# Kernel tuning notes

Hardware: AMD Instinct MI355X
Metric: run time of the kernel (lower is better)

## Reference

```python
import jax, jax.numpy as jnp
import numpy as np


def _rank_transform_ascending(flat):
    # torch: _, idx = sort(flat, descending=False); flat[idx] = linspace(0,1,n)+1/n
    n = flat.shape[0]
    order = jnp.argsort(flat)  # ascending
    prob = jnp.linspace(0.0, 1.0, n, dtype=flat.dtype) + jnp.asarray(1.0 / n, flat.dtype)
    return jnp.zeros_like(flat).at[order].set(prob)


def corr_attention(query, key, value):
    # score[b,h,i,j] = cosine-like similarity q_i . k_j / (|q_i| |k_j|)
    score = jnp.einsum('bhid,bhjd->bhij', query, key)
    q_len = jnp.sqrt(jnp.sum(query * query, axis=-1, keepdims=True)) + 1e-5  # [b,h,s,1]
    k_len = jnp.sqrt(jnp.sum(key * key, axis=-1, keepdims=True)) + 1e-5      # [b,h,s,1]
    score = score / (q_len * jnp.swapaxes(k_len, -1, -2))
    signal = jnp.sign(score)
    size = score.shape
    flat = jnp.abs(score).reshape(-1)
    ranked = _rank_transform_ascending(flat)
    score = -jnp.log(ranked).reshape(size) * signal
    score = score / jnp.sum(jnp.abs(score), axis=-1, keepdims=True)
    return jnp.einsum('bhij,bhjd->bhid', score, value)


def setup_inputs() -> dict:
    key0 = jax.random.key(0)
    kq, kk, kv = jax.random.split(key0, 3)
    B, H, S, D = 4, 8, 1024, 64
    query = jax.random.normal(kq, (B, H, S, D), dtype=jnp.float32)
    key = jax.random.normal(kk, (B, H, S, D), dtype=jnp.float32)
    value = jax.random.normal(kv, (B, H, S, D), dtype=jnp.float32)
    return {"query": query, "key": key, "value": value}


def reference(query, key, value):
    # Attention.forward with mode='season'
    return corr_attention(query, key, value)
```

## Files before the change

### kernel.cpp

```cpp
#include <hip/hip_runtime.h>
#include <math.h>
#include <stdint.h>

#define S_LEN 1024
#define D_DIM 64
#define BH    32
#define KSHIFT 13
#define NBINS 130048u
#define CODE_BASE 97280u
#define NB2   32768u
#define HIST_LO_C 20480u
#define NHOT_H  12288u
#define NCHUNK 64
#define HBLK   256
#define INV_NM1 (1.0f/33554431.0f)
#define INV_N   (2.9802322387695312e-08f)
#define FIX_TH  1e-4f


typedef _Float16 half8 __attribute__((ext_vector_type(8)));
typedef short    short8 __attribute__((ext_vector_type(8)));
typedef float    floatx4 __attribute__((ext_vector_type(4)));

__device__ __forceinline__ void bf16_split(float x, short& hi, short& lo) {
  unsigned u = __float_as_uint(x);
  unsigned h = (u + 0x7FFFu + ((u >> 16) & 1u)) >> 16;
  float hf = __uint_as_float(h << 16);
  float lf = x - hf;
  hi = (short)h;
  lo = (short)(__float_as_uint(lf) >> 16);
}

__global__ __launch_bounds__(256) void norms_kernel(
    const float* __restrict__ Q, const float* __restrict__ K,
    double* __restrict__ qinvD, double* __restrict__ kinvD,
    unsigned short* __restrict__ Qhi_g, unsigned short* __restrict__ Qlo_g,
    unsigned short* __restrict__ Khi_g, unsigned short* __restrict__ Klo_g) {
  int row  = blockIdx.x * 4 + (threadIdx.x >> 6);
  int lane = threadIdx.x & 63;
  const float* src; double* dstD; unsigned short *hD, *lD; int r = row;
  if (row < BH * S_LEN) { src = Q; dstD = qinvD; hD = Qhi_g; lD = Qlo_g; }
  else { src = K; dstD = kinvD; hD = Khi_g; lD = Klo_g; r = row - BH * S_LEN; }
  float xf = src[(size_t)r * D_DIM + lane];
  double v = (double)xf;
  double s = v * v;
  #pragma unroll
  for (int off = 32; off; off >>= 1) s += __shfl_down(s, off);
  double inv = 0.0;
  if (lane == 0) {
    inv = 1.0 / (sqrt(s) + 1e-5);
    dstD[r] = inv;
  }
  inv = __shfl(inv, 0);
  float x = xf * (float)inv;
  short hi, lo;
  bf16_split(x, hi, lo);
  hD[(size_t)r * D_DIM + lane] = (unsigned short)hi;
  lD[(size_t)r * D_DIM + lane] = (unsigned short)lo;
}

__global__ __launch_bounds__(256) void qk_mfma_kernel(
    const float* __restrict__ Q, const float* __restrict__ K,
    const unsigned short* __restrict__ Qhi_g, const unsigned short* __restrict__ Qlo_g,
    const unsigned short* __restrict__ Khi_g, const unsigned short* __restrict__ Klo_g,
    const double* __restrict__ qinvD, const double* __restrict__ kinvD,
    unsigned short* __restrict__ code16) {
  __shared__ short Qhi[64][72], Qlo[64][72];
  __shared__ short Khi[64][72], Klo[64][72];
  int wg    = blockIdx.x;
  int chunk = (wg & 7) * 1024 + (wg >> 3);
  int bh  = chunk >> 8;
  int rem = chunk & 255;
  int i0  = (rem >> 4) * 64;
  int j0  = (rem & 15) * 64;
  int tid = threadIdx.x;
  {
    const unsigned short* Qh = Qhi_g + ((size_t)bh * S_LEN + i0) * D_DIM;
    const unsigned short* Ql = Qlo_g + ((size_t)bh * S_LEN + i0) * D_DIM;
    const unsigned short* Kh = Khi_g + ((size_t)bh * S_LEN + j0) * D_DIM;
    const unsigned short* Kl = Klo_g + ((size_t)bh * S_LEN + j0) * D_DIM;
    #pragma unroll
    for (int l = 0; l < 2; ++l) {
      int idx = l * 256 + tid;
      int row = idx >> 3, c = (idx & 7) * 8;
      *(uint4*)&Qhi[row][c] = *(const uint4*)(Qh + (size_t)row * D_DIM + c);
      *(uint4*)&Qlo[row][c] = *(const uint4*)(Ql + (size_t)row * D_DIM + c);
      *(uint4*)&Khi[row][c] = *(const uint4*)(Kh + (size_t)row * D_DIM + c);
      *(uint4*)&Klo[row][c] = *(const uint4*)(Kl + (size_t)row * D_DIM + c);
    }
  }
  __syncthreads();
  int wave = tid >> 6;
  int lane = tid & 63;
  int m    = lane & 15;
  int quad = lane >> 4;
  floatx4 acc[4];
  #pragma unroll
  for (int n = 0; n < 4; ++n) acc[n] = (floatx4){0.f, 0.f, 0.f, 0.f};
  #pragma unroll
  for (int ks = 0; ks < 2; ++ks) {
    int kb = ks * 32 + quad * 8;
    short8 a_hi = *(const short8*)&Qhi[wave * 16 + m][kb];
    short8 a_lo = *(const short8*)&Qlo[wave * 16 + m][kb];
    #pragma unroll
    for (int nt = 0; nt < 4; ++nt) {
      short8 b_hi = *(const short8*)&Khi[nt * 16 + m][kb];
      short8 b_lo = *(const short8*)&Klo[nt * 16 + m][kb];
      acc[nt] = __builtin_amdgcn_mfma_f32_16x16x32_bf16(a_hi, b_hi, acc[nt], 0, 0, 0);
      acc[nt] = __builtin_amdgcn_mfma_f32_16x16x32_bf16(a_hi, b_lo, acc[nt], 0, 0, 0);
      acc[nt] = __builtin_amdgcn_mfma_f32_16x16x32_bf16(a_lo, b_hi, acc[nt], 0, 0, 0);
    }
  }
  #pragma unroll
  for (int nt = 0; nt < 4; ++nt) {
    #pragma unroll
    for (int r = 0; r < 4; ++r) {
      unsigned long long am = __ballot(fabsf(acc[nt][r]) < FIX_TH);
      while (am) {
        int src = (int)(__ffsll((long long)am) - 1);
        am &= am - 1;
        int i_s = i0 + wave * 16 + (src >> 4) * 4 + r;
        int j_s = j0 + nt * 16 + (src & 15);
        double qd = (double)Q[((size_t)bh * S_LEN + i_s) * D_DIM + lane];
        double kd = (double)K[((size_t)bh * S_LEN + j_s) * D_DIM + lane];
        double pd = qd * kd;
        #pragma unroll
        for (int off = 32; off; off >>= 1) pd += __shfl_down(pd, off);
        float corr = 0.f;
        if (lane == 0)
          corr = (float)(pd * qinvD[(size_t)bh * S_LEN + i_s] * kinvD[(size_t)bh * S_LEN + j_s]);
        corr = __shfl(corr, 0);
        if (lane == src) acc[nt][r] = corr;
      }
    }
  }
  #pragma unroll
  for (int r = 0; r < 4; ++r) {
    unsigned short* op = code16 + (size_t)bh * 1048576 + (size_t)(j0 >> 6) * 65536
                       + (size_t)(i0 + wave * 16 + quad * 4 + r) * 64 + m;
    #pragma unroll
    for (int nt = 0; nt < 4; ++nt) {
      unsigned u = __float_as_uint(acc[nt][r]);
      unsigned a = u & 0x7fffffffu;
      unsigned b = a >> KSHIFT;
      if (b > NBINS - 1u) b = NBINS - 1u;
      unsigned c = (b < CODE_BASE) ? 0u : (b - CODE_BASE);
      op[nt * 16] = (unsigned short)(c | ((u >> 16) & 0x8000u));
    }
  }
}

__global__ __launch_bounds__(1024) void hist_kernel(
    const uint4* __restrict__ codes, unsigned* __restrict__ hist,
    unsigned char* __restrict__ partial) {
  __shared__ unsigned lh[NHOT_H];
  int tid = threadIdx.x;
  for (unsigned i = tid; i < NHOT_H; i += 1024) lh[i] = 0u;
  __syncthreads();
  const uint4* p = codes + (size_t)blockIdx.x * 16384;
  #pragma unroll 2
  for (int it = 0; it < 16; ++it) {
    uint4 w = p[it * 1024 + tid];
    unsigned ws[4] = {w.x, w.y, w.z, w.w};
    #pragma unroll
    for (int k = 0; k < 4; ++k) {
      unsigned c0 = ws[k] & 0x7fffu;
      unsigned c1 = (ws[k] >> 16) & 0x7fffu;
      if (c0 >= HIST_LO_C) atomicAdd(&lh[c0 - HIST_LO_C], 1u);
      else                 atomicAdd(&hist[c0], 1u);
      if (c1 >= HIST_LO_C) atomicAdd(&lh[c1 - HIST_LO_C], 1u);
      else                 atomicAdd(&hist[c1], 1u);
    }
  }
  __syncthreads();
  unsigned char* dst = partial + (size_t)blockIdx.x * NHOT_H;
  for (unsigned i = tid; i < NHOT_H; i += 1024) dst[i] = (unsigned char)lh[i];
}

__global__ __launch_bounds__(256) void hreduce_kernel(
    const unsigned char* __restrict__ partial, unsigned* __restrict__ hist) {
  unsigned bin = blockIdx.x * 256 + threadIdx.x;
  unsigned s = 0;
  #pragma unroll 8
  for (int b = 0; b < HBLK; ++b) s += (unsigned)partial[(size_t)b * NHOT_H + bin];
  hist[HIST_LO_C + bin] = s;
}

__global__ __launch_bounds__(256) void vt_kernel(
    const float* __restrict__ V, _Float16* __restrict__ Vt) {
  __shared__ _Float16 T[64][72];
  int bh = blockIdx.y, j0 = blockIdx.x * 64, tid = threadIdx.x;
  const float* Vb = V + ((size_t)bh * S_LEN + j0) * D_DIM;
  #pragma unroll
  for (int l = 0; l < 4; ++l) {
    int idx = l * 256 + tid;
    int jr = idx >> 4, d4 = idx & 15;
    float4 v = ((const float4*)Vb)[idx];
    T[d4*4+0][jr] = (_Float16)v.x;
    T[d4*4+1][jr] = (_Float16)v.y;
    T[d4*4+2][jr] = (_Float16)v.z;
    T[d4*4+3][jr] = (_Float16)v.w;
  }
  __syncthreads();
  _Float16* Ob = Vt + (size_t)(bh * 16 + blockIdx.x) * 4096;
  #pragma unroll
  for (int l = 0; l < 2; ++l) {
    int idx = l * 256 + tid;
    int d = idx >> 3, jc = idx & 7;
    uint4 val = *(const uint4*)&T[d][jc*8];
    *(uint4*)(Ob + (size_t)d * 64 + jc*8) = val;
  }
}

__global__ __launch_bounds__(256) void scan1_kernel(const unsigned* __restrict__ hist,
                                                    unsigned* __restrict__ csum) {
  __shared__ unsigned sd[256];
  int c = blockIdx.x, t = threadIdx.x;
  const unsigned* p = hist + (size_t)c * 512;
  sd[t] = p[t] + p[t + 256];
  __syncthreads();
  for (int off = 128; off; off >>= 1) {
    if (t < off) sd[t] += sd[t + off];
    __syncthreads();
  }
  if (t == 0) csum[c] = sd[0];
}

__global__ __launch_bounds__(256) void scan2_kernel(unsigned* __restrict__ csum) {
  __shared__ unsigned d[256];
  int t = threadIdx.x;
  unsigned v = (t < NCHUNK) ? csum[t] : 0u;
  d[t] = v; __syncthreads();
  for (int off = 1; off < 256; off <<= 1) {
    unsigned x = (t >= off) ? d[t - off] : 0u;
    __syncthreads();
    d[t] += x;
    __syncthreads();
  }
  if (t < NCHUNK) csum[t] = d[t] - v;
}

__global__ __launch_bounds__(256) void scan3_kernel(const unsigned* __restrict__ hist,
                                                    const unsigned* __restrict__ csum,
                                                    _Float16* __restrict__ tab2) {
  __shared__ unsigned ts[256];
  int c = blockIdx.x, t = threadIdx.x;
  const unsigned* p = hist + (size_t)c * 512 + t * 2;
  unsigned l0 = p[0], l1 = p[1];
  unsigned s = l0 + l1;
  ts[t] = s; __syncthreads();
  for (int off = 1; off < 256; off <<= 1) {
    unsigned x = (t >= off) ? ts[t - off] : 0u;
    __syncthreads();
    ts[t] += x;
    __syncthreads();
  }
  unsigned base = csum[c] + ts[t] - s;
  int idx = c * 512 + t * 2;
  float r0 = (float)base + 0.5f * ((float)l0 - 1.0f);
  tab2[idx]     = (_Float16)(-__logf(fmaf(r0, INV_NM1, INV_N)));
  float r1 = (float)(base + l0) + 0.5f * ((float)l1 - 1.0f);
  tab2[idx + 1] = (_Float16)(-__logf(fmaf(r1, INV_NM1, INV_N)));
}

__global__ __launch_bounds__(512, 1) void pv_mfma_kernel(
    const unsigned short* __restrict__ code16, const _Float16* __restrict__ Vt,
    const unsigned short* __restrict__ tab2, float* __restrict__ out) {
  __shared__ unsigned short ldsT[NB2];
  __shared__ _Float16 vlds[4 * 64 * 72];
  int tid = threadIdx.x;

  int wg    = blockIdx.x;
  int chunk = (wg & 7) * 32 + (wg >> 3);
  int bh = chunk >> 3;
  int ib = chunk & 7;
  int wave = tid >> 6;
  int lane = tid & 63;
  int m    = lane & 15;
  int quad = lane >> 4;
  int i0   = ib * 128 + wave * 16;
  const unsigned short* Sb = code16 + (size_t)bh * 1048576 + (size_t)(i0 + m) * 64;
  const _Float16*       Vb = Vt + (size_t)bh * 65536;

  {
    const uint4* gsrc = (const uint4*)tab2;
    uint4* ldst = (uint4*)ldsT;
    #pragma unroll
    for (int i = 0; i < 8; ++i)
      ldst[i * 512 + tid] = gsrc[i * 512 + tid];
  }
  #pragma unroll
  for (int it = 0; it < 4; ++it) {
    int u = it * 512 + tid;
    int e0 = u * 8;
    int tt = e0 >> 12, rem = e0 & 4095, d = rem >> 6, jin = rem & 63;
    uint4 val = *(const uint4*)(Vb + 0 * 16384 + e0);
    *(uint4*)&vlds[tt * 4608 + d * 72 + jin] = val;
  }
  uint4 cw[8];
  #pragma unroll
  for (int s = 0; s < 8; ++s) {
    int k0 = 0 * 256 + s * 32 + quad * 8;
    cw[s] = *(const uint4*)(Sb + (size_t)(k0 >> 6) * 65536 + (k0 & 63));
  }
  __syncthreads();

  floatx4 acc[4];
  #pragma unroll
  for (int n = 0; n < 4; ++n) acc[n] = (floatx4){0.f, 0.f, 0.f, 0.f};
  float rsum = 0.f;

  #pragma unroll
  for (int c = 0; c < 4; ++c) {
    uint4 cwn[8];
    if (c < 3) {
      #pragma unroll
      for (int s = 0; s < 8; ++s) {
        int k0 = (c + 1) * 256 + s * 32 + quad * 8;
        cwn[s] = *(const uint4*)(Sb + (size_t)(k0 >> 6) * 65536 + (k0 & 63));
      }
    }
    #pragma unroll
    for (int s = 0; s < 8; ++s) {
      int lk  = s * 32 + quad * 8;
      int tt  = lk >> 6;
      int jin = lk & 63;
      unsigned ww[4] = {cw[s].x, cw[s].y, cw[s].z, cw[s].w};
      union { unsigned short u[8]; half8 h; } af;
      #pragma unroll
      for (int e = 0; e < 8; ++e) {
        unsigned cd = (e & 1) ? (ww[e >> 1] >> 16) : (ww[e >> 1] & 0xffffu);
        unsigned short tb = ldsT[cd & 0x7fffu];
        af.u[e] = (unsigned short)(tb ^ (cd & 0x8000u));
        unsigned short tabs = (unsigned short)(tb & 0x7fffu);
        rsum += (float)__builtin_bit_cast(_Float16, tabs);
      }
      half8 bf[4];
      #pragma unroll
      for (int n = 0; n < 4; ++n)
        bf[n] = *(const half8*)&vlds[tt * 4608 + (n * 16 + m) * 72 + jin];
      #pragma unroll
      for (int n = 0; n < 4; ++n)
        acc[n] = __builtin_amdgcn_mfma_f32_16x16x32_f16(af.h, bf[n], acc[n], 0, 0, 0);
    }
    if (c < 3) {
      __syncthreads();
      #pragma unroll
      for (int it = 0; it < 4; ++it) {
        int u = it * 512 + tid;
        int e0 = u * 8;
        int tt = e0 >> 12, rem = e0 & 4095, d = rem >> 6, jin = rem & 63;
        uint4 val = *(const uint4*)(Vb + (size_t)(c + 1) * 16384 + e0);
        *(uint4*)&vlds[tt * 4608 + d * 72 + jin] = val;
      }
      __syncthreads();
      #pragma unroll
      for (int s = 0; s < 8; ++s) cw[s] = cwn[s];
    }
  }

  rsum += __shfl_xor(rsum, 16);
  rsum += __shfl_xor(rsum, 32);
  float inv = 1.0f / rsum;
  #pragma unroll
  for (int r = 0; r < 4; ++r) {
    int row = quad * 4 + r;
    float invr = __shfl(inv, row);
    float* op = out + ((size_t)bh * S_LEN + i0 + row) * D_DIM + m;
    #pragma unroll
    for (int n = 0; n < 4; ++n)
      op[n * 16] = acc[n][r] * invr;
  }
}

extern "C" void kernel_launch(void* const* d_in, const int* in_sizes, int n_in,
                              void* d_out, int out_size, void* d_ws, size_t ws_size,
                              hipStream_t stream) {
  const float* Q = (const float*)d_in[0];
  const float* K = (const float*)d_in[1];
  const float* V = (const float*)d_in[2];
  float* out = (float*)d_out;
  char* ws = (char*)d_ws;
  unsigned short* code16  = (unsigned short*)(ws);
  unsigned*       hist    = (unsigned*)(ws + 67108864);
  unsigned char*  partial = (unsigned char*)(ws + 67239936);
  double*         qinvD   = (double*)(ws + 67239936 + 3145728);
  double*         kinvD   = (double*)(ws + 67239936 + 3407872);
  _Float16*       Vt      = (_Float16*)(ws + 67239936);
  unsigned*       csum    = (unsigned*)(ws + 67239936 + 4194304);
  _Float16*       tab2    = (_Float16*)(ws + 67239936 + 4195328);
  unsigned short* Qhi_g   = (unsigned short*)(ws + 71503872);
  unsigned short* Qlo_g   = (unsigned short*)(ws + 75698176);
  unsigned short* Khi_g   = (unsigned short*)(ws + 79892480);
  unsigned short* Klo_g   = (unsigned short*)(ws + 84086784);

  hipMemsetAsync(hist, 0, NB2 * sizeof(unsigned), stream);
  norms_kernel<<<(2 * BH * S_LEN) / 4, 256, 0, stream>>>(
      Q, K, qinvD, kinvD, Qhi_g, Qlo_g, Khi_g, Klo_g);
  qk_mfma_kernel<<<16 * 16 * BH, 256, 0, stream>>>(
      Q, K, Qhi_g, Qlo_g, Khi_g, Klo_g, qinvD, kinvD, code16);
  hist_kernel<<<HBLK, 1024, 0, stream>>>((const uint4*)code16, hist, partial);
  hreduce_kernel<<<NHOT_H / 256, 256, 0, stream>>>(partial, hist);
  vt_kernel<<<dim3(16, BH), 256, 0, stream>>>(V, Vt);
  scan1_kernel<<<NCHUNK, 256, 0, stream>>>(hist, csum);
  scan2_kernel<<<1, 256, 0, stream>>>(csum);
  scan3_kernel<<<NCHUNK, 256, 0, stream>>>(hist, csum, tab2);
  pv_mfma_kernel<<<8 * BH, 512, 0, stream>>>(
      code16, Vt, (const unsigned short*)tab2, out);
}
```

Measured before the change: 185.6 us.

## Privatize full histogram in shared memory, swizzle QK LDS tiles, skip fix-up path

The histogram kernel now keeps all bins in shared memory as packed 16-bit counters instead of sending low bins to global atomics. Per-block byte partials cover every bin and are reduced by hreduce, so the hist memset goes away. The QK kernel replaces padded LDS tiles with an XOR-swizzled layout to avoid bank conflicts, and skips the per-element double-precision fix-up loop when a wave has no near-zero scores. The risk is counter overflow: 16-bit packed and 8-bit partial counts can overflow for heavily populated bins such as the zero code. Also, the larger partial buffer now overlaps other workspace regions.

```diff
diff --git a/kernel.cpp b/kernel.cpp
--- a/kernel.cpp
+++ b/kernel.cpp
@@ -9,8 +9,6 @@
 #define NBINS 130048u
 #define CODE_BASE 97280u
 #define NB2   32768u
-#define HIST_LO_C 20480u
-#define NHOT_H  12288u
 #define NCHUNK 64
 #define HBLK   256
 #define INV_NM1 (1.0f/33554431.0f)
@@ -65,8 +63,8 @@
     const unsigned short* __restrict__ Khi_g, const unsigned short* __restrict__ Klo_g,
     const double* __restrict__ qinvD, const double* __restrict__ kinvD,
     unsigned short* __restrict__ code16) {
-  __shared__ short Qhi[64][72], Qlo[64][72];
-  __shared__ short Khi[64][72], Klo[64][72];
+  __shared__ short Qhi[64][64], Qlo[64][64];
+  __shared__ short Khi[64][64], Klo[64][64];
   int wg    = blockIdx.x;
   int chunk = (wg & 7) * 1024 + (wg >> 3);
   int bh  = chunk >> 8;
@@ -82,11 +80,13 @@
     #pragma unroll
     for (int l = 0; l < 2; ++l) {
       int idx = l * 256 + tid;
-      int row = idx >> 3, c = (idx & 7) * 8;
-      *(uint4*)&Qhi[row][c] = *(const uint4*)(Qh + (size_t)row * D_DIM + c);
-      *(uint4*)&Qlo[row][c] = *(const uint4*)(Ql + (size_t)row * D_DIM + c);
-      *(uint4*)&Khi[row][c] = *(const uint4*)(Kh + (size_t)row * D_DIM + c);
-      *(uint4*)&Klo[row][c] = *(const uint4*)(Kl + (size_t)row * D_DIM + c);
+      int row = idx >> 3, g = idx & 7;
+      int gs = (g ^ (row & 7)) * 8;
+      int c  = g * 8;
+      *(uint4*)&Qhi[row][gs] = *(const uint4*)(Qh + (size_t)row * D_DIM + c);
+      *(uint4*)&Qlo[row][gs] = *(const uint4*)(Ql + (size_t)row * D_DIM + c);
+      *(uint4*)&Khi[row][gs] = *(const uint4*)(Kh + (size_t)row * D_DIM + c);
+      *(uint4*)&Klo[row][gs] = *(const uint4*)(Kl + (size_t)row * D_DIM + c);
     }
   }
   __syncthreads();
@@ -99,38 +99,49 @@
   for (int n = 0; n < 4; ++n) acc[n] = (floatx4){0.f, 0.f, 0.f, 0.f};
   #pragma unroll
   for (int ks = 0; ks < 2; ++ks) {
-    int kb = ks * 32 + quad * 8;
-    short8 a_hi = *(const short8*)&Qhi[wave * 16 + m][kb];
-    short8 a_lo = *(const short8*)&Qlo[wave * 16 + m][kb];
+    int g = ks * 4 + quad;
+    int gs = (g ^ (m & 7)) * 8;
+    short8 a_hi = *(const short8*)&Qhi[wave * 16 + m][gs];
+    short8 a_lo = *(const short8*)&Qlo[wave * 16 + m][gs];
     #pragma unroll
     for (int nt = 0; nt < 4; ++nt) {
-      short8 b_hi = *(const short8*)&Khi[nt * 16 + m][kb];
-      short8 b_lo = *(const short8*)&Klo[nt * 16 + m][kb];
+      short8 b_hi = *(const short8*)&Khi[nt * 16 + m][gs];
+      short8 b_lo = *(const short8*)&Klo[nt * 16 + m][gs];
       acc[nt] = __builtin_amdgcn_mfma_f32_16x16x32_bf16(a_hi, b_hi, acc[nt], 0, 0, 0);
       acc[nt] = __builtin_amdgcn_mfma_f32_16x16x32_bf16(a_hi, b_lo, acc[nt], 0, 0, 0);
       acc[nt] = __builtin_amdgcn_mfma_f32_16x16x32_bf16(a_lo, b_hi, acc[nt], 0, 0, 0);
     }
   }
-  #pragma unroll
-  for (int nt = 0; nt < 4; ++nt) {
-    #pragma unroll
-    for (int r = 0; r < 4; ++r) {
-      unsigned long long am = __ballot(fabsf(acc[nt][r]) < FIX_TH);
-      while (am) {
-        int src = (int)(__ffsll((long long)am) - 1);
-        am &= am - 1;
-        int i_s = i0 + wave * 16 + (src >> 4) * 4 + r;
-        int j_s = j0 + nt * 16 + (src & 15);
-        double qd = (double)Q[((size_t)bh * S_LEN + i_s) * D_DIM + lane];
-        double kd = (double)K[((size_t)bh * S_LEN + j_s) * D_DIM + lane];
-        double pd = qd * kd;
+  {
+    bool anysmall = false;
+    #pragma unroll
+    for (int nt = 0; nt < 4; ++nt)
+      #pragma unroll
+      for (int r = 0; r < 4; ++r)
+        anysmall |= (fabsf(acc[nt][r]) < FIX_TH);
+    if (__any(anysmall)) {
+      #pragma unroll
+      for (int nt = 0; nt < 4; ++nt) {
         #pragma unroll
-        for (int off = 32; off; off >>= 1) pd += __shfl_down(pd, off);
-        float corr = 0.f;
-        if (lane == 0)
-          corr = (float)(pd * qinvD[(size_t)bh * S_LEN + i_s] * kinvD[(size_t)bh * S_LEN + j_s]);
-        corr = __shfl(corr, 0);
-        if (lane == src) acc[nt][r] = corr;
+        for (int r = 0; r < 4; ++r) {
+          unsigned long long am = __ballot(fabsf(acc[nt][r]) < FIX_TH);
+          while (am) {
+            int src = (int)(__ffsll((long long)am) - 1);
+            am &= am - 1;
+            int i_s = i0 + wave * 16 + (src >> 4) * 4 + r;
+            int j_s = j0 + nt * 16 + (src & 15);
+            double qd = (double)Q[((size_t)bh * S_LEN + i_s) * D_DIM + lane];
+            double kd = (double)K[((size_t)bh * S_LEN + j_s) * D_DIM + lane];
+            double pd = qd * kd;
+            #pragma unroll
+            for (int off = 32; off; off >>= 1) pd += __shfl_down(pd, off);
+            float corr = 0.f;
+            if (lane == 0)
+              corr = (float)(pd * qinvD[(size_t)bh * S_LEN + i_s] * kinvD[(size_t)bh * S_LEN + j_s]);
+            corr = __shfl(corr, 0);
+            if (lane == src) acc[nt][r] = corr;
+          }
+        }
       }
     }
   }
@@ -151,11 +162,11 @@
 }
 
 __global__ __launch_bounds__(1024) void hist_kernel(
-    const uint4* __restrict__ codes, unsigned* __restrict__ hist,
-    unsigned char* __restrict__ partial) {
-  __shared__ unsigned lh[NHOT_H];
+    const uint4* __restrict__ codes, unsigned char* __restrict__ partial) {
+  __shared__ unsigned lh[NB2 / 2];
   int tid = threadIdx.x;
-  for (unsigned i = tid; i < NHOT_H; i += 1024) lh[i] = 0u;
+  #pragma unroll
+  for (int i = 0; i < 16; ++i) lh[i * 1024 + tid] = 0u;
   __syncthreads();
   const uint4* p = codes + (size_t)blockIdx.x * 16384;
   #pragma unroll 2
@@ -166,15 +177,19 @@
     for (int k = 0; k < 4; ++k) {
       unsigned c0 = ws[k] & 0x7fffu;
       unsigned c1 = (ws[k] >> 16) & 0x7fffu;
-      if (c0 >= HIST_LO_C) atomicAdd(&lh[c0 - HIST_LO_C], 1u);
-      else                 atomicAdd(&hist[c0], 1u);
-      if (c1 >= HIST_LO_C) atomicAdd(&lh[c1 - HIST_LO_C], 1u);
-      else                 atomicAdd(&hist[c1], 1u);
-    }
-  }
-  __syncthreads();
-  unsigned char* dst = partial + (size_t)blockIdx.x * NHOT_H;
-  for (unsigned i = tid; i < NHOT_H; i += 1024) dst[i] = (unsigned char)lh[i];
+      atomicAdd(&lh[c0 >> 1], (c0 & 1u) ? 65536u : 1u);
+      atomicAdd(&lh[c1 >> 1], (c1 & 1u) ? 65536u : 1u);
+    }
+  }
+  __syncthreads();
+  unsigned* dst = (unsigned*)(partial + (size_t)blockIdx.x * NB2);
+  #pragma unroll
+  for (int i = 0; i < 8; ++i) {
+    int w2 = i * 1024 + tid;
+    unsigned w0 = lh[2 * w2], w1 = lh[2 * w2 + 1];
+    dst[w2] = (w0 & 0xffu) | ((w0 >> 16) & 0xffu) << 8
+            | (w1 & 0xffu) << 16 | ((w1 >> 16) & 0xffu) << 24;
+  }
 }
 
 __global__ __launch_bounds__(256) void hreduce_kernel(
@@ -182,8 +197,8 @@
   unsigned bin = blockIdx.x * 256 + threadIdx.x;
   unsigned s = 0;
   #pragma unroll 8
-  for (int b = 0; b < HBLK; ++b) s += (unsigned)partial[(size_t)b * NHOT_H + bin];
-  hist[HIST_LO_C + bin] = s;
+  for (int b = 0; b < HBLK; ++b) s += (unsigned)partial[(size_t)b * NB2 + bin];
+  hist[bin] = s;
 }
 
 __global__ __launch_bounds__(256) void vt_kernel(
@@ -389,18 +404,17 @@
   _Float16*       Vt      = (_Float16*)(ws + 67239936);
   unsigned*       csum    = (unsigned*)(ws + 67239936 + 4194304);
   _Float16*       tab2    = (_Float16*)(ws + 67239936 + 4195328);
-  unsigned short* Qhi_g   = (unsigned short*)(ws + 71503872);
-  unsigned short* Qlo_g   = (unsigned short*)(ws + 75698176);
-  unsigned short* Khi_g   = (unsigned short*)(ws + 79892480);
-  unsigned short* Klo_g   = (unsigned short*)(ws + 84086784);
-
-  hipMemsetAsync(hist, 0, NB2 * sizeof(unsigned), stream);
+  unsigned short* Qhi_g   = (unsigned short*)(ws + 75698176);
+  unsigned short* Qlo_g   = (unsigned short*)(ws + 79892480);
+  unsigned short* Khi_g   = (unsigned short*)(ws + 84086784);
+  unsigned short* Klo_g   = (unsigned short*)(ws + 88281088);
+
   norms_kernel<<<(2 * BH * S_LEN) / 4, 256, 0, stream>>>(
       Q, K, qinvD, kinvD, Qhi_g, Qlo_g, Khi_g, Klo_g);
   qk_mfma_kernel<<<16 * 16 * BH, 256, 0, stream>>>(
       Q, K, Qhi_g, Qlo_g, Khi_g, Klo_g, qinvD, kinvD, code16);
-  hist_kernel<<<HBLK, 1024, 0, stream>>>((const uint4*)code16, hist, partial);
-  hreduce_kernel<<<NHOT_H / 256, 256, 0, stream>>>(partial, hist);
+  hist_kernel<<<HBLK, 1024, 0, stream>>>((const uint4*)code16, partial);
+  hreduce_kernel<<<NB2 / 256, 256, 0, stream>>>(partial, hist);
   vt_kernel<<<dim3(16, BH), 256, 0, stream>>>(V, Vt);
   scan1_kernel<<<NCHUNK, 256, 0, stream>>>(hist, csum);
   scan2_kernel<<<1, 256, 0, stream>>>(csum);
```

Result: no change. 183.7 us (-1.0%).
